# Performance work log

Measured on AMD Instinct MI355X. Metric: run time of the kernel, lower is better.

The kernel has to match this reference:

```python
import jax, jax.numpy as jnp
import numpy as np

EMB_DIM = 512
CATE1_CNT = 10
VOCAB = 100000
H_D = 1024
BN_EPS = 1e-5
NEG = -1e30  # masked value for max-pool


def setup_inputs() -> dict:
    key = jax.random.key(0)
    ks = jax.random.split(key, 12)
    B, LT, LD = 1024, 50, 200
    title = jax.random.randint(ks[0], (B, LT), 0, VOCAB, dtype=jnp.int64)
    desc = jax.random.randint(ks[1], (B, LD), 0, VOCAB, dtype=jnp.int64)
    t_len = jax.random.randint(ks[2], (B,), 1, LT + 1, dtype=jnp.int64)
    d_len = jax.random.randint(ks[3], (B,), 1, LD + 1, dtype=jnp.int64)
    emb = jax.random.normal(ks[4], (VOCAB, EMB_DIM), dtype=jnp.float32) * 0.02
    W_fc = jax.random.normal(ks[5], (4 * EMB_DIM, H_D), dtype=jnp.float32) * (1.0 / np.sqrt(4 * EMB_DIM))
    b_fc = jnp.zeros((H_D,), dtype=jnp.float32)
    gamma = jnp.ones((H_D,), dtype=jnp.float32)
    beta = jnp.zeros((H_D,), dtype=jnp.float32)
    W_clf = jax.random.normal(ks[6], (H_D, CATE1_CNT), dtype=jnp.float32) * (1.0 / np.sqrt(H_D))
    b_clf = jnp.zeros((CATE1_CNT,), dtype=jnp.float32)
    return {"title": title, "desc": desc, "t_len": t_len, "d_len": d_len,
            "emb": emb, "W_fc": W_fc, "b_fc": b_fc, "gamma": gamma,
            "beta": beta, "W_clf": W_clf, "b_clf": b_clf}


def _swem_pool(tokens, lens, emb):
    # tokens: [B, L] int, lens: [B] int -> (avg, max) each [B, D]
    e = emb[tokens]                                   # [B, L, D] gather
    L = tokens.shape[1]
    mask = (jnp.arange(L)[None, :] < lens[:, None])[..., None]  # [B, L, 1]
    s = jnp.sum(jnp.where(mask, e, 0.0), axis=1)      # [B, D]
    avg = s / jnp.maximum(lens, 1).astype(e.dtype)[:, None]
    mx = jnp.max(jnp.where(mask, e, NEG), axis=1)     # [B, D]
    return avg, mx


def reference(title, desc, t_len, d_len, emb, W_fc, b_fc, gamma, beta, W_clf, b_clf):
    t_avg, t_max = _swem_pool(title, t_len, emb)
    d_avg, d_max = _swem_pool(desc, d_len, emb)
    swem = jnp.concatenate([t_avg, t_max, d_avg, d_max], axis=-1)  # [B, 2048]
    h = swem @ W_fc + b_fc                                         # [B, H_D]
    # BatchNorm1d in training mode: batch statistics
    mean = jnp.mean(h, axis=0)
    var = jnp.var(h, axis=0)
    h = (h - mean) * jax.lax.rsqrt(var + BN_EPS) * gamma + beta
    h = jax.nn.relu(h)
    return h @ W_clf + b_clf                                       # [B, 10]
```

## Files before the change

### kernel.cpp

```cpp
#include <hip/hip_runtime.h>
#include <hip/hip_bf16.h>

#define EMB_DIM 512
#define B_SZ 1024
#define LT 50
#define LD 200
#define H_D 1024
#define K_FC 2048
#define NCLS 10
#define BN_EPS 1e-5f
#define NEGV -1e30f

typedef short short8 __attribute__((ext_vector_type(8)));
typedef float f32x4 __attribute__((ext_vector_type(4)));

#define SWZ(r, b) ((b) ^ (((r) & 7) << 4))

#define ACC4(S, M, E) \
  S.x += E.x; S.y += E.y; S.z += E.z; S.w += E.w; \
  M.x = fmaxf(M.x, E.x); M.y = fmaxf(M.y, E.y); \
  M.z = fmaxf(M.z, E.z); M.w = fmaxf(M.w, E.w);

__global__ __launch_bounds__(512) void pool_tr_kernel(
    const int* __restrict__ title, const int* __restrict__ desc,
    const int* __restrict__ t_len, const int* __restrict__ d_len,
    const float* __restrict__ emb, __hip_bfloat16* __restrict__ swem,
    const float* __restrict__ W, __hip_bfloat16* __restrict__ Wt,
    const float* __restrict__ Wclf, float* __restrict__ WclfT) {
  __shared__ float sm[8192];
  __shared__ int idxs[264];

  const int bid = blockIdx.x;
  const int tid = threadIdx.x;

  if (bid >= 2 * B_SZ) {
    const int t = bid - 2 * B_SZ;
    if (t == 512) {
      for (int idx = tid; idx < NCLS * H_D; idx += 512) {
        int j = idx >> 10, k = idx & 1023;
        WclfT[j * H_D + k] = Wclf[(size_t)k * NCLS + j];
      }
      return;
    }
    const int n0 = (t & 15) * 64;
    const int k0 = (t >> 4) * 64;
#pragma unroll
    for (int i = 0; i < 8; ++i) {
      int idx = i * 512 + tid;
      int r = idx >> 6, c = idx & 63;
      sm[r * 65 + c] = W[(size_t)(k0 + r) * H_D + n0 + c];
    }
    __syncthreads();
#pragma unroll
    for (int i = 0; i < 8; ++i) {
      int idx = i * 512 + tid;
      int r = idx >> 6, c = idx & 63;
      Wt[(size_t)(n0 + r) * K_FC + k0 + c] = __float2bfloat16(sm[c * 65 + r]);
    }
    return;
  }

  const int b = bid >> 1;
  const int half = bid & 1;
  const int wave = tid >> 6;
  const int lane = tid & 63;
  const int dbase = half * 256 + lane * 4;

  if (tid < LT) idxs[tid] = title[b * LT + tid];
  else if (tid >= 64 && tid < 64 + LD) idxs[tid] = desc[b * LD + tid - 64];
  const int tl = t_len[b];
  const int dl = d_len[b];
  __syncthreads();

#define POOL_LIST(LEN, IDXOFF, SARR, MARR)                                         \
  {                                                                                \
    float4 s0 = make_float4(0.f, 0.f, 0.f, 0.f), s1 = s0;                          \
    float4 m0 = make_float4(NEGV, NEGV, NEGV, NEGV), m1 = m0;                      \
    const int cnt = (LEN > wave) ? ((LEN - wave + 7) >> 3) : 0;                    \
    if (cnt >= 2) {                                                                \
      float4 e0 = *reinterpret_cast<const float4*>(                                \
          emb + (size_t)idxs[IDXOFF + wave] * EMB_DIM + dbase);                    \
      float4 e1 = *reinterpret_cast<const float4*>(                                \
          emb + (size_t)idxs[IDXOFF + wave + 8] * EMB_DIM + dbase);                \
      int i = 2;                                                                   \
      for (; i + 1 < cnt; i += 2) {                                                \
        float4 n0 = *reinterpret_cast<const float4*>(                              \
            emb + (size_t)idxs[IDXOFF + wave + i * 8] * EMB_DIM + dbase);          \
        float4 n1 = *reinterpret_cast<const float4*>(                              \
            emb + (size_t)idxs[IDXOFF + wave + (i + 1) * 8] * EMB_DIM + dbase);    \
        ACC4(s0, m0, e0); ACC4(s1, m1, e1);                                        \
        e0 = n0; e1 = n1;                                                          \
      }                                                                            \
      ACC4(s0, m0, e0); ACC4(s1, m1, e1);                                          \
      if (i < cnt) {                                                               \
        float4 t2 = *reinterpret_cast<const float4*>(                              \
            emb + (size_t)idxs[IDXOFF + wave + i * 8] * EMB_DIM + dbase);          \
        ACC4(s0, m0, t2);                                                          \
      }                                                                            \
    } else if (cnt == 1) {                                                         \
      float4 e0 = *reinterpret_cast<const float4*>(                                \
          emb + (size_t)idxs[IDXOFF + wave] * EMB_DIM + dbase);                    \
      ACC4(s0, m0, e0);                                                            \
    }                                                                              \
    s0.x += s1.x; s0.y += s1.y; s0.z += s1.z; s0.w += s1.w;                        \
    m0.x = fmaxf(m0.x, m1.x); m0.y = fmaxf(m0.y, m1.y);                            \
    m0.z = fmaxf(m0.z, m1.z); m0.w = fmaxf(m0.w, m1.w);                            \
    *reinterpret_cast<float4*>(&sm[(SARR * 8 + wave) * 256 + lane * 4]) = s0;      \
    *reinterpret_cast<float4*>(&sm[(MARR * 8 + wave) * 256 + lane * 4]) = m0;      \
  }

  POOL_LIST(tl, 0, 0, 1)
  POOL_LIST(dl, 64, 2, 3)

  __syncthreads();

  if (tid < 64) {
    const float it = 1.0f / (float)tl;
    const float id = 1.0f / (float)dl;
    float4 ts = make_float4(0.f, 0.f, 0.f, 0.f);
    float4 tm = make_float4(NEGV, NEGV, NEGV, NEGV);
    float4 ds = make_float4(0.f, 0.f, 0.f, 0.f);
    float4 dm = make_float4(NEGV, NEGV, NEGV, NEGV);
#pragma unroll
    for (int w = 0; w < 8; ++w) {
      float4 a = *reinterpret_cast<const float4*>(&sm[(0 * 8 + w) * 256 + tid * 4]);
      ts.x += a.x; ts.y += a.y; ts.z += a.z; ts.w += a.w;
      float4 bmx = *reinterpret_cast<const float4*>(&sm[(1 * 8 + w) * 256 + tid * 4]);
      tm.x = fmaxf(tm.x, bmx.x); tm.y = fmaxf(tm.y, bmx.y);
      tm.z = fmaxf(tm.z, bmx.z); tm.w = fmaxf(tm.w, bmx.w);
      float4 c = *reinterpret_cast<const float4*>(&sm[(2 * 8 + w) * 256 + tid * 4]);
      ds.x += c.x; ds.y += c.y; ds.z += c.z; ds.w += c.w;
      float4 dmx = *reinterpret_cast<const float4*>(&sm[(3 * 8 + w) * 256 + tid * 4]);
      dm.x = fmaxf(dm.x, dmx.x); dm.y = fmaxf(dm.y, dmx.y);
      dm.z = fmaxf(dm.z, dmx.z); dm.w = fmaxf(dm.w, dmx.w);
    }
    __hip_bfloat16* row = swem + (size_t)b * K_FC + half * 256 + tid * 4;
    union { ushort4 v; __hip_bfloat16 h[4]; } u;
    u.h[0] = __float2bfloat16(ts.x * it); u.h[1] = __float2bfloat16(ts.y * it);
    u.h[2] = __float2bfloat16(ts.z * it); u.h[3] = __float2bfloat16(ts.w * it);
    *reinterpret_cast<ushort4*>(&row[0 * EMB_DIM]) = u.v;
    u.h[0] = __float2bfloat16(tm.x); u.h[1] = __float2bfloat16(tm.y);
    u.h[2] = __float2bfloat16(tm.z); u.h[3] = __float2bfloat16(tm.w);
    *reinterpret_cast<ushort4*>(&row[1 * EMB_DIM]) = u.v;
    u.h[0] = __float2bfloat16(ds.x * id); u.h[1] = __float2bfloat16(ds.y * id);
    u.h[2] = __float2bfloat16(ds.z * id); u.h[3] = __float2bfloat16(ds.w * id);
    *reinterpret_cast<ushort4*>(&row[2 * EMB_DIM]) = u.v;
    u.h[0] = __float2bfloat16(dm.x); u.h[1] = __float2bfloat16(dm.y);
    u.h[2] = __float2bfloat16(dm.z); u.h[3] = __float2bfloat16(dm.w);
    *reinterpret_cast<ushort4*>(&row[3 * EMB_DIM]) = u.v;
  }
}

__global__ __launch_bounds__(512) void gemm_mfma_kernel(
    const __hip_bfloat16* __restrict__ A,
    const __hip_bfloat16* __restrict__ Bt,
    const float* __restrict__ bias, float* __restrict__ C,
    float* __restrict__ psum, float* __restrict__ psq) {
  __shared__ unsigned char As[2][8192];
  __shared__ unsigned char Bs[2][8192];
  __shared__ float reds[2][4][16];
  __shared__ float redq[2][4][16];
  const int tid = threadIdx.x;
  const int lane = tid & 63;
  const int wave = tid >> 6;
  const int wr = wave >> 2;
  const int wc = wave & 3;
  const int m0 = blockIdx.y * 64, n0 = blockIdx.x * 64;

  f32x4 acc[2] = {};

  const int rs = tid >> 3;
  const int os = tid & 7;
  const int hi = lane >> 4;
  const int lo = lane & 15;

  const __hip_bfloat16* pa = A + (size_t)(m0 + rs) * K_FC + os * 8;
  const __hip_bfloat16* pb = Bt + (size_t)(n0 + rs) * K_FC + os * 8;
  const int swz = SWZ(rs, rs * 128 + os * 16);

  float4 a1 = *reinterpret_cast<const float4*>(pa);
  float4 b1 = *reinterpret_cast<const float4*>(pb);
  *reinterpret_cast<float4*>(&As[0][swz]) = a1;
  *reinterpret_cast<float4*>(&Bs[0][swz]) = b1;
  a1 = *reinterpret_cast<const float4*>(pa + 64);
  b1 = *reinterpret_cast<const float4*>(pb + 64);
  __syncthreads();

  int cur = 0;
  for (int k0 = 0; k0 < K_FC; k0 += 64) {
    float4 an = make_float4(0.f, 0.f, 0.f, 0.f), bn = an;
    if (k0 + 128 < K_FC) {
      an = *reinterpret_cast<const float4*>(pa + k0 + 128);
      bn = *reinterpret_cast<const float4*>(pb + k0 + 128);
    }

#pragma unroll
    for (int kks = 0; kks < 2; ++kks) {
      short8 af[2];
#pragma unroll
      for (int mi = 0; mi < 2; ++mi) {
        int r = wr * 32 + mi * 16 + lo;
        af[mi] = *reinterpret_cast<const short8*>(&As[cur][SWZ(r, r * 128 + kks * 64 + hi * 16)]);
      }
      int rb = wc * 16 + lo;
      short8 bf = *reinterpret_cast<const short8*>(&Bs[cur][SWZ(rb, rb * 128 + kks * 64 + hi * 16)]);
#pragma unroll
      for (int mi = 0; mi < 2; ++mi)
        acc[mi] = __builtin_amdgcn_mfma_f32_16x16x32_bf16(af[mi], bf, acc[mi], 0, 0, 0);
    }

    if (k0 + 64 < K_FC) {
      *reinterpret_cast<float4*>(&As[cur ^ 1][swz]) = a1;
      *reinterpret_cast<float4*>(&Bs[cur ^ 1][swz]) = b1;
    }
    __syncthreads();
    a1 = an; b1 = bn;
    cur ^= 1;
  }

  {
    int col = n0 + wc * 16 + lo;
    float bv = bias[col];
    float s = 0.f, q = 0.f;
#pragma unroll
    for (int mi = 0; mi < 2; ++mi) {
#pragma unroll
      for (int r = 0; r < 4; ++r) {
        float v = acc[mi][r] + bv;
        s += v; q += v * v;
        int rowm = m0 + wr * 32 + mi * 16 + hi * 4 + r;
        C[(size_t)rowm * H_D + col] = v;
      }
    }
    s += __shfl_xor(s, 16);
    s += __shfl_xor(s, 32);
    q += __shfl_xor(q, 16);
    q += __shfl_xor(q, 32);
    if (lane < 16) { reds[wr][wc][lo] = s; redq[wr][wc][lo] = q; }
  }
  __syncthreads();
  if (tid < 64) {
    int wc2 = tid >> 4, lo2 = tid & 15;
    float s = reds[0][wc2][lo2] + reds[1][wc2][lo2];
    float q = redq[0][wc2][lo2] + redq[1][wc2][lo2];
    psum[blockIdx.y * H_D + n0 + tid] = s;
    psq[blockIdx.y * H_D + n0 + tid] = q;
  }
}

__global__ __launch_bounds__(256) void bn_final_kernel(
    const float* __restrict__ psum, const float* __restrict__ psq,
    const float* __restrict__ gamma, const float* __restrict__ beta,
    float* __restrict__ scale, float* __restrict__ shift) {
  const int col = blockIdx.x * 256 + threadIdx.x;
  float s = 0.f, q = 0.f;
#pragma unroll
  for (int i = 0; i < 16; ++i) {
    s += psum[i * H_D + col];
    q += psq[i * H_D + col];
  }
  const float inv_n = 1.0f / (float)B_SZ;
  float mean = s * inv_n;
  float var = q * inv_n - mean * mean;
  float rstd = rsqrtf(var + BN_EPS);
  float sc = rstd * gamma[col];
  scale[col] = sc;
  shift[col] = beta[col] - mean * sc;
}

__global__ __launch_bounds__(256) void clf_kernel(
    const float* __restrict__ h, const float* __restrict__ scale,
    const float* __restrict__ shift, const float* __restrict__ WT,
    const float* __restrict__ bclf, float* __restrict__ out) {
  __shared__ float v[H_D];
  const int row = blockIdx.x;
  const int tid = threadIdx.x;
#pragma unroll
  for (int i = 0; i < 4; ++i) {
    int k = tid + i * 256;
    float x = h[(size_t)row * H_D + k] * scale[k] + shift[k];
    v[k] = fmaxf(x, 0.f);
  }
  __syncthreads();
  const int wave = tid >> 6, lane = tid & 63;
  for (int j = wave; j < NCLS; j += 4) {
    const float* wrow = WT + j * H_D;
    float acc = 0.f;
#pragma unroll
    for (int i = 0; i < 16; ++i) {
      int k = lane + i * 64;
      acc += v[k] * wrow[k];
    }
#pragma unroll
    for (int off = 32; off > 0; off >>= 1) acc += __shfl_down(acc, off, 64);
    if (lane == 0) out[(size_t)row * NCLS + j] = acc + bclf[j];
  }
}

extern "C" void kernel_launch(void* const* d_in, const int* in_sizes, int n_in,
                              void* d_out, int out_size, void* d_ws, size_t ws_size,
                              hipStream_t stream) {
  const int* title = (const int*)d_in[0];
  const int* desc  = (const int*)d_in[1];
  const int* t_len = (const int*)d_in[2];
  const int* d_len = (const int*)d_in[3];
  const float* emb   = (const float*)d_in[4];
  const float* W_fc  = (const float*)d_in[5];
  const float* b_fc  = (const float*)d_in[6];
  const float* gamma = (const float*)d_in[7];
  const float* beta  = (const float*)d_in[8];
  const float* W_clf = (const float*)d_in[9];
  const float* b_clf = (const float*)d_in[10];
  float* out = (float*)d_out;

  unsigned char* ws = (unsigned char*)d_ws;
  __hip_bfloat16* swem = (__hip_bfloat16*)ws;
  __hip_bfloat16* Wt   = (__hip_bfloat16*)(ws + (4u << 20));
  float* h     = (float*)(ws + (8u << 20));
  float* psum  = (float*)(ws + (12u << 20));
  float* psq   = psum + 16 * H_D;
  float* scale = psq + 16 * H_D;
  float* shift = scale + H_D;
  float* WclfT = shift + H_D;

  const int n_tr_blocks = (K_FC / 64) * (H_D / 64) + 1;
  pool_tr_kernel<<<2 * B_SZ + n_tr_blocks, 512, 0, stream>>>(
      title, desc, t_len, d_len, emb, swem, W_fc, Wt, W_clf, WclfT);
  gemm_mfma_kernel<<<dim3(H_D / 64, B_SZ / 64), 512, 0, stream>>>(swem, Wt, b_fc, h, psum, psq);
  bn_final_kernel<<<H_D / 256, 256, 0, stream>>>(psum, psq, gamma, beta, scale, shift);
  clf_kernel<<<B_SZ, 256, 0, stream>>>(h, scale, shift, WclfT, b_clf, out);
}
```

Measured before the change: 64.31 us.

## Fuse BN finalize into GEMM via last-block atomic counter and swizzle block order

Removes the separate bn_final kernel launch: each GEMM block publishes its partial column sums, increments a global atomic counter, and the last block to finish computes the BN scale/shift. The counter is reset by an extra block in the pooling kernel. GEMM block indices are also remapped so that consecutive blocks spread across different tiles for better cache locality. This saves one launch, at the cost of a serial tail where a single block reduces all 1024 columns, plus a dependence on fences for correctness.

```diff
diff --git a/kernel.cpp b/kernel.cpp
--- a/kernel.cpp
+++ b/kernel.cpp
@@ -26,7 +26,8 @@
     const int* __restrict__ t_len, const int* __restrict__ d_len,
     const float* __restrict__ emb, __hip_bfloat16* __restrict__ swem,
     const float* __restrict__ W, __hip_bfloat16* __restrict__ Wt,
-    const float* __restrict__ Wclf, float* __restrict__ WclfT) {
+    const float* __restrict__ Wclf, float* __restrict__ WclfT,
+    int* __restrict__ counter) {
   __shared__ float sm[8192];
   __shared__ int idxs[264];
 
@@ -35,6 +36,10 @@
 
   if (bid >= 2 * B_SZ) {
     const int t = bid - 2 * B_SZ;
+    if (t == 513) {
+      if (tid == 0) *counter = 0;
+      return;
+    }
     if (t == 512) {
       for (int idx = tid; idx < NCLS * H_D; idx += 512) {
         int j = idx >> 10, k = idx & 1023;
@@ -155,17 +160,25 @@
     const __hip_bfloat16* __restrict__ A,
     const __hip_bfloat16* __restrict__ Bt,
     const float* __restrict__ bias, float* __restrict__ C,
-    float* __restrict__ psum, float* __restrict__ psq) {
+    float* __restrict__ psum, float* __restrict__ psq,
+    const float* __restrict__ gamma, const float* __restrict__ beta,
+    float* __restrict__ scale, float* __restrict__ shift,
+    int* __restrict__ counter) {
   __shared__ unsigned char As[2][8192];
   __shared__ unsigned char Bs[2][8192];
   __shared__ float reds[2][4][16];
   __shared__ float redq[2][4][16];
+  __shared__ int lastflag;
   const int tid = threadIdx.x;
   const int lane = tid & 63;
   const int wave = tid >> 6;
   const int wr = wave >> 2;
   const int wc = wave & 3;
-  const int m0 = blockIdx.y * 64, n0 = blockIdx.x * 64;
+
+  const int lin = blockIdx.y * 16 + blockIdx.x;
+  const int swzb = (lin & 7) * 32 + (lin >> 3);
+  const int bx = swzb & 15, by = swzb >> 4;
+  const int m0 = by * 64, n0 = bx * 64;
 
   f32x4 acc[2] = {};
 
@@ -243,29 +256,32 @@
     int wc2 = tid >> 4, lo2 = tid & 15;
     float s = reds[0][wc2][lo2] + reds[1][wc2][lo2];
     float q = redq[0][wc2][lo2] + redq[1][wc2][lo2];
-    psum[blockIdx.y * H_D + n0 + tid] = s;
-    psq[blockIdx.y * H_D + n0 + tid] = q;
-  }
-}
-
-__global__ __launch_bounds__(256) void bn_final_kernel(
-    const float* __restrict__ psum, const float* __restrict__ psq,
-    const float* __restrict__ gamma, const float* __restrict__ beta,
-    float* __restrict__ scale, float* __restrict__ shift) {
-  const int col = blockIdx.x * 256 + threadIdx.x;
-  float s = 0.f, q = 0.f;
-#pragma unroll
-  for (int i = 0; i < 16; ++i) {
-    s += psum[i * H_D + col];
-    q += psq[i * H_D + col];
-  }
-  const float inv_n = 1.0f / (float)B_SZ;
-  float mean = s * inv_n;
-  float var = q * inv_n - mean * mean;
-  float rstd = rsqrtf(var + BN_EPS);
-  float sc = rstd * gamma[col];
-  scale[col] = sc;
-  shift[col] = beta[col] - mean * sc;
+    psum[by * H_D + n0 + tid] = s;
+    psq[by * H_D + n0 + tid] = q;
+  }
+
+  __threadfence();
+  __syncthreads();
+  if (tid == 0) lastflag = (atomicAdd(counter, 1) == 255);
+  __syncthreads();
+  if (lastflag) {
+    __threadfence();
+    for (int col = tid; col < H_D; col += 512) {
+      float s = 0.f, q = 0.f;
+#pragma unroll
+      for (int i = 0; i < 16; ++i) {
+        s += psum[i * H_D + col];
+        q += psq[i * H_D + col];
+      }
+      const float inv_n = 1.0f / (float)B_SZ;
+      float mean = s * inv_n;
+      float var = q * inv_n - mean * mean;
+      float rstd = rsqrtf(var + BN_EPS);
+      float sc = rstd * gamma[col];
+      scale[col] = sc;
+      shift[col] = beta[col] - mean * sc;
+    }
+  }
 }
 
 __global__ __launch_bounds__(256) void clf_kernel(
@@ -322,11 +338,12 @@
   float* scale = psq + 16 * H_D;
   float* shift = scale + H_D;
   float* WclfT = shift + H_D;
-
-  const int n_tr_blocks = (K_FC / 64) * (H_D / 64) + 1;
+  int*   counter = (int*)(WclfT + NCLS * H_D);
+
+  const int n_tr_blocks = (K_FC / 64) * (H_D / 64) + 2;
   pool_tr_kernel<<<2 * B_SZ + n_tr_blocks, 512, 0, stream>>>(
-      title, desc, t_len, d_len, emb, swem, W_fc, Wt, W_clf, WclfT);
-  gemm_mfma_kernel<<<dim3(H_D / 64, B_SZ / 64), 512, 0, stream>>>(swem, Wt, b_fc, h, psum, psq);
-  bn_final_kernel<<<H_D / 256, 256, 0, stream>>>(psum, psq, gamma, beta, scale, shift);
+      title, desc, t_len, d_len, emb, swem, W_fc, Wt, W_clf, WclfT, counter);
+  gemm_mfma_kernel<<<dim3(16, 16), 512, 0, stream>>>(
+      swem, Wt, b_fc, h, psum, psq, gamma, beta, scale, shift, counter);
   clf_kernel<<<B_SZ, 256, 0, stream>>>(h, scale, shift, WclfT, b_clf, out);
 }
```

New measurement: 105.9 us. 64.7% more time.
